# Optimization experiments

Measured on AMD Instinct MI355X. Metric: run time of the kernel, lower is better.

## Reference

```python
import jax, jax.numpy as jnp
import numpy as np

N, E, R, L = 20000, 160000, 3, 2
IN, HID, H, OUT = 64, 128, 16, 1
FH = HID // H   # per-head dim = 8
HD2 = HID // 2  # MLP bottleneck = 64


def setup_inputs() -> dict:
    key = jax.random.key(0)
    ks = iter(jax.random.split(key, 40))
    def w(*shape):
        return jax.random.normal(next(ks), shape, jnp.float32) * 0.05
    inp = dict(
        inputs=jax.random.normal(next(ks), (N, IN), jnp.float32),
        src=jax.random.randint(next(ks), (R, E), 0, N, dtype=jnp.int32),
        dst=jax.random.randint(next(ks), (R, E), 0, N, dtype=jnp.int32),
        e1_W=w(IN, HID), e1_b=jnp.zeros(HID), e_g=jnp.ones(HID), e_bt=jnp.zeros(HID),
        e2_W=w(HID, HID), e2_b=jnp.zeros(HID),
        gat_W=w(L, R, HID, HID), gat_al=w(L, R, H, FH), gat_ar=w(L, R, H, FH),
        gat_b=jnp.zeros((L, R, HID)),
        attn_p=w(L, R, HID),
        m1_W=w(L, HID, HD2), m1_b=jnp.zeros((L, HD2)), m_g=jnp.ones((L, HD2)), m_bt=jnp.zeros((L, HD2)),
        m2_W=w(L, HD2, HID), m2_b=jnp.zeros((L, HID)),
        d1_W=w(HID, HD2), d1_b=jnp.zeros(HD2), d_g=jnp.ones(HD2), d_bt=jnp.zeros(HD2),
        d2_W=w(HD2, OUT), d2_b=jnp.zeros(OUT),
    )
    return inp


def _bn(x, g, b):
    # BatchNorm1d, training mode: biased batch statistics, eps=1e-5
    mu = x.mean(0)
    var = jnp.mean((x - mu) ** 2, 0)
    return g * (x - mu) * jax.lax.rsqrt(var + 1e-5) + b


def _mlp(x, W1, b1, g, bt, W2, b2, skip=False):
    h = jax.nn.relu(_bn(x @ W1 + b1, g, bt))
    o = h @ W2 + b2
    return o + h if skip else o


def _gat(x, W, al, ar, b, src, dst):
    # single-relation DGL GATConv (feat_drop=attn_drop=0, neg_slope=0.2, bias)
    z = (x @ W).reshape(N, H, FH)                 # [N,H,FH]
    el = (z * al).sum(-1)                          # [N,H]
    er = (z * ar).sum(-1)                          # [N,H]
    e = jax.nn.leaky_relu(el[src] + er[dst], 0.2)  # [E,H]
    m = jax.ops.segment_max(e, dst, num_segments=N)
    m = jnp.where(jnp.isfinite(m), m, 0.0)
    ex = jnp.exp(e - m[dst])
    s = jax.ops.segment_sum(ex, dst, num_segments=N)
    alpha = ex / s[dst]                            # edge softmax over in-edges
    out = jax.ops.segment_sum(alpha[:, :, None] * z[src], dst, num_segments=N)
    return out.reshape(N, HID) + b                 # flatten heads + bias


def reference(inputs, src, dst, e1_W, e1_b, e_g, e_bt, e2_W, e2_b,
              gat_W, gat_al, gat_ar, gat_b, attn_p,
              m1_W, m1_b, m_g, m_bt, m2_W, m2_b,
              d1_W, d1_b, d_g, d_bt, d2_W, d2_b):
    h = _mlp(inputs, e1_W, e1_b, e_g, e_bt, e2_W, e2_b, skip=True)  # embed, skip
    gat_v = jax.vmap(_gat, in_axes=(None, 0, 0, 0, 0, 0, 0))        # over relations
    for l in range(L):
        stacked = gat_v(h, gat_W[l], gat_al[l], gat_ar[l], gat_b[l], src, dst)  # [R,N,HID]
        w = jax.nn.softmax(attn_p[l], axis=0)        # per-dim softmax over relations [R,HID]
        v = jnp.einsum('rnf,rf->nf', stacked, w)     # attn-weighted relation agg
        h = _mlp(v, m1_W[l], m1_b[l], m_g[l], m_bt[l], m2_W[l], m2_b[l]) + h
    return _mlp(h, d1_W, d1_b, d_g, d_bt, d2_W, d2_b)
```

## Files before the change

### kernel.cpp

```cpp
#include <hip/hip_runtime.h>
#include <math.h>

constexpr int kN   = 20000;
constexpr int kE   = 160000;
constexpr int kR   = 3;
constexpr int kL   = 2;
constexpr int kIN  = 64;
constexpr int kHID = 128;
constexpr int kH   = 16;
constexpr int kFH  = 8;
constexpr int kHD2 = 64;

typedef __bf16 bf16x8 __attribute__((ext_vector_type(8)));
typedef float  f32x4  __attribute__((ext_vector_type(4)));

__device__ __forceinline__ bf16x8 ldfrag(const __bf16* p) {
  return __builtin_bit_cast(bf16x8, *(const uint4*)p);
}
__device__ __forceinline__ f32x4 MF(bf16x8 a, bf16x8 b, f32x4 c) {
  return __builtin_amdgcn_mfma_f32_16x16x32_bf16(a, b, c, 0, 0, 0);
}

__device__ __forceinline__ void splitrow(const float* __restrict__ p, int koff,
                                         bool bn, const float* scS, const float* shS,
                                         bf16x8& hi, bf16x8& lo) {
  float4 xa = *(const float4*)(p + koff);
  float4 xb = *(const float4*)(p + koff + 4);
  float x[8] = {xa.x, xa.y, xa.z, xa.w, xb.x, xb.y, xb.z, xb.w};
  union { __bf16 b[8]; bf16x8 v; } uh, ul;
#pragma unroll
  for (int e = 0; e < 8; e++) {
    float y = x[e];
    if (bn) y = fmaxf(fmaf(y, scS[koff + e], shS[koff + e]), 0.f);
    __bf16 hb = (__bf16)y;
    uh.b[e] = hb;
    ul.b[e] = (__bf16)(y - (float)hb);
  }
  hi = uh.v; lo = ul.v;
}

template <int BP>
__global__ __launch_bounds__(256) void mgemm_kernel(
    const float* __restrict__ A, const __bf16* __restrict__ WT,
    const float* __restrict__ bias, const float* __restrict__ resf, int resmode,
    const float* __restrict__ bnstat, const float* __restrict__ bng,
    const float* __restrict__ bnbt, float invn,
    float* __restrict__ statS,
    float* __restrict__ Cf, __bf16* __restrict__ Chi,
    const float* __restrict__ alb, const float* __restrict__ arb,
    float* __restrict__ elb, float* __restrict__ erb,
    int n, int k, int m, long wstride, long cstride) {
  __shared__ __bf16 Bh[64][136];
  __shared__ __bf16 Bl[(BP == 3) ? 64 : 1][136];
  __shared__ float scS[128], shS[128];
  const int t  = threadIdx.x;
  const int w  = t >> 6;
  const int l  = t & 63;
  const int lr = l & 15;
  const int lg = l >> 4;
  const int rb = blockIdx.x * 64 + w * 16;
  const int c0 = blockIdx.y * 64;
  const __bf16* Whi = WT + (size_t)blockIdx.z * wstride;
  const __bf16* Wlo = Whi + (size_t)k * m;
  if (Chi) Chi += (size_t)blockIdx.z * cstride;
  const float* al = alb ? alb + blockIdx.z * kHID : nullptr;
  const float* ar = arb ? arb + blockIdx.z * kHID : nullptr;
  if (elb) { elb += blockIdx.z * 16; erb += blockIdx.z * 16; }

  const bool bn = bnstat != nullptr;
  if (bn && t < k) {
    float mu  = bnstat[t] * invn;
    float var = bnstat[k + t] * invn - mu * mu;
    float s = bng[t] * rsqrtf(var + 1e-5f);
    scS[t] = s; shS[t] = bnbt[t] - mu * s;
  }
  const int kseg = k >> 3;
  for (int idx = t; idx < 64 * kseg; idx += 256) {
    int col = idx / kseg, seg = idx - col * kseg;
    *(uint4*)&Bh[col][seg * 8] = *(const uint4*)&Whi[(size_t)(c0 + col) * k + seg * 8];
    if constexpr (BP == 3)
      *(uint4*)&Bl[col][seg * 8] = *(const uint4*)&Wlo[(size_t)(c0 + col) * k + seg * 8];
  }
  __syncthreads();

  int r0 = rb + lr; if (r0 > n - 1) r0 = n - 1;
  f32x4 acc[4] = {};

  for (int ks = 0; ks < (k >> 5); ks++) {
    const int koff = ks * 32 + lg * 8;
    bf16x8 a0h, a0l;
    splitrow(&A[(size_t)r0 * k], koff, bn, scS, shS, a0h, a0l);
#pragma unroll
    for (int j = 0; j < 4; j++) {
      bf16x8 bh = ldfrag(&Bh[j * 16 + lr][koff]);
      acc[j] = MF(a0h, bh, acc[j]);
      acc[j] = MF(a0l, bh, acc[j]);
      if constexpr (BP == 3) {
        bf16x8 bl = ldfrag(&Bl[j * 16 + lr][koff]);
        acc[j] = MF(a0h, bl, acc[j]);
      }
    }
  }

  float s[4] = {}, s2[4] = {};
#pragma unroll
  for (int q = 0; q < 4; q++) {
    int row = rb + lg * 4 + q;
    bool ok = row < n;
#pragma unroll
    for (int j = 0; j < 4; j++) {
      int col = c0 + j * 16 + lr;
      float v = acc[j][q];
      if (bias) v += bias[col];
      size_t off = (size_t)row * m + col;
      if (ok) {
        if (resmode == 1) v += resf[off];
        else if (resmode == 2) v += fmaxf(fmaf(resf[off], scS[col], shS[col]), 0.f);
        if (Cf) Cf[off] = v;
        if (Chi) Chi[off] = (__bf16)v;
        s[j] += v; s2[j] += v * v;
      }
    }
  }
  if (statS) {
    __syncthreads();
    float* red = (float*)&Bh[0][0];
#pragma unroll
    for (int j = 0; j < 4; j++) {
      float a = s[j], b = s2[j];
      a += __shfl_xor(a, 16, 64); a += __shfl_xor(a, 32, 64);
      b += __shfl_xor(b, 16, 64); b += __shfl_xor(b, 32, 64);
      if (lg == 0) { red[w * 64 + j * 16 + lr] = a; red[256 + w * 64 + j * 16 + lr] = b; }
    }
    __syncthreads();
    if (t < 64) {
      float a = red[t] + red[64 + t] + red[128 + t] + red[192 + t];
      float b = red[256 + t] + red[320 + t] + red[384 + t] + red[448 + t];
      atomicAdd(&statS[c0 + t], a);
      atomicAdd(&statS[m + c0 + t], b);
    }
  }
  if (al) {
#pragma unroll
    for (int q = 0; q < 4; q++) {
      int row = rb + lg * 4 + q;
#pragma unroll
      for (int j = 0; j < 4; j++) {
        int col = c0 + j * 16 + lr;
        float zv = acc[j][q];
        float pl = zv * al[col];
        float pr = zv * ar[col];
        pl += __shfl_xor(pl, 1, 64); pl += __shfl_xor(pl, 2, 64); pl += __shfl_xor(pl, 4, 64);
        pr += __shfl_xor(pr, 1, 64); pr += __shfl_xor(pr, 2, 64); pr += __shfl_xor(pr, 4, 64);
        if ((lr & 7) == 0 && row < n) {
          int hd = col >> 3;
          elb[((size_t)row << 6) + hd] = pl;
          erb[((size_t)row << 6) + hd] = pr;
        }
      }
    }
  }
}

struct WDesc { const float* src; long doff; int k, m; };
struct WDescs { WDesc d[13]; };
__global__ void prep_kernel(WDescs ds, __bf16* __restrict__ wt,
                            const int* __restrict__ dst, int* __restrict__ deg) {
  int y = blockIdx.y;
  if (y < 13) {
    WDesc dd = ds.d[y];
    int idx = blockIdx.x * 256 + threadIdx.x;
    if (idx >= dd.k * dd.m) return;
    int row = idx / dd.m, col = idx - row * dd.m;
    float v = dd.src[idx];
    __bf16 hb = (__bf16)v;
    __bf16 lb = (__bf16)(v - (float)hb);
    wt[dd.doff + (size_t)col * dd.k + row] = hb;
    wt[dd.doff + (size_t)dd.k * dd.m + (size_t)col * dd.k + row] = lb;
  } else {
    int r = y - 13;
    int e = blockIdx.x * 256 + threadIdx.x;
    if (e < kE) atomicAdd(&deg[r * kN + dst[r * kE + e]], 1);
  }
}

__global__ __launch_bounds__(1024) void csr_scan_kernel(const int* __restrict__ deg,
                                                        int* __restrict__ rowptr) {
  const int r = blockIdx.y;
  const int* dg = deg + r * kN;
  int* rp = rowptr + r * (kN + 1);
  const int t = threadIdx.x;
  constexpr int C = (kN + 1023) / 1024;
  const int base = t * C;
  int sum = 0;
#pragma unroll
  for (int i = 0; i < C; i++) {
    int j = base + i;
    if (j < kN) sum += dg[j];
  }
  __shared__ int warpTot[16];
  int lane = t & 63, wid = t >> 6;
  int v = sum;
  for (int off = 1; off < 64; off <<= 1) {
    int y = __shfl_up(v, off, 64);
    if (lane >= off) v += y;
  }
  if (lane == 63) warpTot[wid] = v;
  __syncthreads();
  int wadd = 0;
#pragma unroll
  for (int i = 0; i < 16; i++) if (i < wid) wadd += warpTot[i];
  int run = wadd + v - sum;
#pragma unroll
  for (int i = 0; i < C; i++) {
    int j = base + i;
    if (j < kN) { rp[j] = run; run += dg[j]; }
  }
  if (t == 1023) rp[kN] = run;
}

__global__ void scatter_kernel(const int* __restrict__ src, const int* __restrict__ dst,
                               const int* __restrict__ rowptr, int* __restrict__ cursor,
                               int* __restrict__ col) {
  int r = blockIdx.y;
  int e = blockIdx.x * 256 + threadIdx.x;
  if (e < kE) {
    int d = dst[r * kE + e];
    int p = atomicAdd(&cursor[r * kN + d], 1);
    col[r * kE + rowptr[r * (kN + 1) + d] + p] = src[r * kE + e];
  }
}

__global__ void gat3_kernel(const int* __restrict__ rowptr, const int* __restrict__ colidx,
                            const ushort* __restrict__ z, const float* __restrict__ elb,
                            const float* __restrict__ erb,
                            const float* __restrict__ attn_pl, const float* __restrict__ gat_bl,
                            float* __restrict__ vv) {
  __shared__ float wsmS[kR * kHID], cvecS[kHID];
  int t = threadIdx.x;
  if (t < kHID) {
    float p0 = attn_pl[t], p1 = attn_pl[kHID + t], p2 = attn_pl[2 * kHID + t];
    float mx = fmaxf(p0, fmaxf(p1, p2));
    float e0 = __expf(p0 - mx), e1 = __expf(p1 - mx), e2 = __expf(p2 - mx);
    float si = 1.f / (e0 + e1 + e2);
    wsmS[t] = e0 * si; wsmS[kHID + t] = e1 * si; wsmS[2 * kHID + t] = e2 * si;
    cvecS[t] = (e0 * gat_bl[t] + e1 * gat_bl[kHID + t] + e2 * gat_bl[2 * kHID + t]) * si;
  }
  __syncthreads();
  int idx = blockIdx.x * 256 + t;
  if (idx >= kN * kH) return;
  int d = idx >> 4, hh = idx & 15;
  const int fo = hh << 3;
  float out[kFH];
#pragma unroll
  for (int f = 0; f < kFH; f++) out[f] = cvecS[fo + f];
  for (int r = 0; r < kR; r++) {
    const int* rp = rowptr + r * (kN + 1);
    const int* ci = colidx + (size_t)r * kE;
    const ushort* zr = z + (size_t)r * kN * kHID;
    const int ro = r * 16 + hh;
    float erd = erb[((size_t)d << 6) + ro];
    int beg = rp[d], end = rp[d + 1];
    float s = 0.f;
    float acc[kFH] = {};
    for (int p = beg; p < end; p += 8) {
      int q[8]; float ev[8]; uint4 zz[8];
#pragma unroll
      for (int u = 0; u < 8; u++) {
        int pp = p + u;
        q[u] = ci[pp < end ? pp : end - 1];
      }
#pragma unroll
      for (int u = 0; u < 8; u++) ev[u] = elb[((size_t)q[u] << 6) + ro];
#pragma unroll
      for (int u = 0; u < 8; u++) zz[u] = *(const uint4*)(zr + ((size_t)q[u] << 7) + fo);
#pragma unroll
      for (int u = 0; u < 8; u++) {
        float v = ev[u] + erd;
        v = v > 0.f ? v : 0.2f * v;
        float ex = (p + u < end) ? __expf(v) : 0.f;
        s += ex;
        acc[0] = fmaf(ex, __uint_as_float(zz[u].x << 16),         acc[0]);
        acc[1] = fmaf(ex, __uint_as_float(zz[u].x & 0xffff0000u), acc[1]);
        acc[2] = fmaf(ex, __uint_as_float(zz[u].y << 16),         acc[2]);
        acc[3] = fmaf(ex, __uint_as_float(zz[u].y & 0xffff0000u), acc[3]);
        acc[4] = fmaf(ex, __uint_as_float(zz[u].z << 16),         acc[4]);
        acc[5] = fmaf(ex, __uint_as_float(zz[u].z & 0xffff0000u), acc[5]);
        acc[6] = fmaf(ex, __uint_as_float(zz[u].w << 16),         acc[6]);
        acc[7] = fmaf(ex, __uint_as_float(zz[u].w & 0xffff0000u), acc[7]);
      }
    }
    float inv = s > 0.f ? 1.f / s : 0.f;
    const float* wp = wsmS + r * kHID + fo;
#pragma unroll
    for (int f = 0; f < kFH; f++) out[f] = fmaf(wp[f] * inv, acc[f], out[f]);
  }
  float4* vp = (float4*)(vv + ((size_t)d << 7) + fo);
  vp[0] = make_float4(out[0], out[1], out[2], out[3]);
  vp[1] = make_float4(out[4], out[5], out[6], out[7]);
}

__global__ void gemv_out_kernel(const float* __restrict__ A, const float* __restrict__ statS,
                                const float* __restrict__ g, const float* __restrict__ bt,
                                float invn, const float* __restrict__ w,
                                const float* __restrict__ b, float* __restrict__ out,
                                int n, int k) {
  __shared__ float scS[kHD2], shS[kHD2];
  int t = threadIdx.x;
  if (t < k) {
    float mu  = statS[t] * invn;
    float var = statS[k + t] * invn - mu * mu;
    float s = g[t] * rsqrtf(var + 1e-5f);
    scS[t] = s; shS[t] = bt[t] - mu * s;
  }
  __syncthreads();
  int i = blockIdx.x * 256 + t;
  if (i >= n) return;
  const float4* a = (const float4*)(A + (size_t)i * k);
  float acc = b[0];
  for (int j4 = 0; j4 < k / 4; j4++) {
    float4 x = a[j4];
    int c = j4 * 4;
    acc = fmaf(fmaxf(fmaf(x.x, scS[c],     shS[c]),     0.f), w[c],     acc);
    acc = fmaf(fmaxf(fmaf(x.y, scS[c + 1], shS[c + 1]), 0.f), w[c + 1], acc);
    acc = fmaf(fmaxf(fmaf(x.z, scS[c + 2], shS[c + 2]), 0.f), w[c + 2], acc);
    acc = fmaf(fmaxf(fmaf(x.w, scS[c + 3], shS[c + 3]), 0.f), w[c + 3], acc);
  }
  out[i] = acc;
}

extern "C" void kernel_launch(void* const* d_in, const int* in_sizes, int n_in,
                              void* d_out, int out_size, void* d_ws, size_t ws_size,
                              hipStream_t stream) {
  const float* inputs = (const float*)d_in[0];
  const int*   src    = (const int*)d_in[1];
  const int*   dst    = (const int*)d_in[2];
  const float* e1_W   = (const float*)d_in[3];
  const float* e1_b   = (const float*)d_in[4];
  const float* e_g    = (const float*)d_in[5];
  const float* e_bt   = (const float*)d_in[6];
  const float* e2_W   = (const float*)d_in[7];
  const float* e2_b   = (const float*)d_in[8];
  const float* gat_W  = (const float*)d_in[9];
  const float* gat_al = (const float*)d_in[10];
  const float* gat_ar = (const float*)d_in[11];
  const float* gat_b  = (const float*)d_in[12];
  const float* attn_p = (const float*)d_in[13];
  const float* m1_W   = (const float*)d_in[14];
  const float* m1_b   = (const float*)d_in[15];
  const float* m_g    = (const float*)d_in[16];
  const float* m_bt   = (const float*)d_in[17];
  const float* m2_W   = (const float*)d_in[18];
  const float* m2_b   = (const float*)d_in[19];
  const float* d1_W   = (const float*)d_in[20];
  const float* d1_b   = (const float*)d_in[21];
  const float* d_g    = (const float*)d_in[22];
  const float* d_bt   = (const float*)d_in[23];
  const float* d2_W   = (const float*)d_in[24];
  const float* d2_b   = (const float*)d_in[25];

  float* ws = (float*)d_ws;
  size_t o = 0;
  float*  h     = ws + o; o += (size_t)kN * kHID;
  float*  bufA  = ws + o; o += (size_t)kN * kHID;
  float*  vv    = ws + o; o += (size_t)kN * kHID;
  float*  elbuf = ws + o; o += (size_t)kN * 64;
  float*  erbuf = ws + o; o += (size_t)kN * 64;
  __bf16* z     = (__bf16*)(ws + o); o += (size_t)kR * kN * kHID / 2;
  __bf16* wt    = (__bf16*)(ws + o); o += 327680 / 2;
  int* degcur   = (int*)(ws + o); o += (size_t)6 * kN;
  float* stats  = ws + o; o += 640;
  int* rowptr   = (int*)(ws + o); o += (size_t)kR * (kN + 1);
  int* colidx   = (int*)(ws + o); o += (size_t)kR * kE;
  (void)ws_size; (void)in_sizes; (void)n_in; (void)out_size;

  int* deg    = degcur;
  int* cursor = degcur + 3 * kN;
  float* stat_e1 = stats;
  float* stat_m1[2] = {stats + 256, stats + 384};
  float* stat_d1 = stats + 512;

  const long kWE1 = 0, kWE2 = 16384, kWZ = 49152;
  const long kWM1_0 = 245760, kWM1_1 = 262144, kWM2_0 = 278528, kWM2_1 = 294912, kWD1 = 311296;

  auto nb = [](long t) { return (int)((t + 255) / 256); };
  const dim3 gE(nb(kE), kR);
  const dim3 gP(nb(kE), 16);
  const dim3 gM128((kN + 63) / 64, 2, 1);
  const dim3 gM64((kN + 63) / 64, 1, 1);
  const dim3 gMZ((kN + 63) / 64, 2, kR);
  const float invn = 1.0f / kN;
  float* F0 = nullptr; const float* cF0 = nullptr;

  WDescs wd;
  wd.d[0] = {e1_W, kWE1, kIN, kHID};
  wd.d[1] = {e2_W, kWE2, kHID, kHID};
  for (int i = 0; i < 6; i++) wd.d[2 + i] = {gat_W + (size_t)i * 16384, kWZ + (long)i * 32768, kHID, kHID};
  wd.d[8]  = {m1_W,        kWM1_0, kHID, kHD2};
  wd.d[9]  = {m1_W + 8192, kWM1_1, kHID, kHD2};
  wd.d[10] = {m2_W,        kWM2_0, kHD2, kHID};
  wd.d[11] = {m2_W + 8192, kWM2_1, kHD2, kHID};
  wd.d[12] = {d1_W,        kWD1,   kHID, kHD2};
  hipMemsetAsync(degcur, 0, ((size_t)6 * kN + 640) * sizeof(int), stream);
  prep_kernel<<<gP, 256, 0, stream>>>(wd, wt, dst, deg);
  csr_scan_kernel<<<dim3(1, kR), 1024, 0, stream>>>(deg, rowptr);
  scatter_kernel<<<gE, 256, 0, stream>>>(src, dst, rowptr, cursor, colidx);

  mgemm_kernel<3><<<gM128, 256, 0, stream>>>(inputs, wt + kWE1, e1_b, cF0, 0,
                                          cF0, cF0, cF0, invn, stat_e1, bufA, nullptr,
                                          cF0, cF0, F0, F0, kN, kIN, kHID, 0, 0);
  mgemm_kernel<3><<<gM128, 256, 0, stream>>>(bufA, wt + kWE2, e2_b, bufA, 2,
                                          stat_e1, e_g, e_bt, invn, F0, h, nullptr,
                                          cF0, cF0, F0, F0, kN, kHID, kHID, 0, 0);

  for (int l = 0; l < kL; l++) {
    mgemm_kernel<2><<<gMZ, 256, 0, stream>>>(h, wt + kWZ + (long)l * 3 * 32768, cF0, cF0, 0,
                                          cF0, cF0, cF0, invn, F0, F0, z,
                                          gat_al + (size_t)l * kR * kHID,
                                          gat_ar + (size_t)l * kR * kHID, elbuf, erbuf,
                                          kN, kHID, kHID, 32768, (long)kN * kHID);
    gat3_kernel<<<nb((long)kN * kH), 256, 0, stream>>>(rowptr, colidx, (const ushort*)z,
                                             elbuf, erbuf,
                                             attn_p + (size_t)l * kR * kHID,
                                             gat_b + (size_t)l * kR * kHID, vv);
    mgemm_kernel<3><<<gM64, 256, 0, stream>>>(vv, wt + (l ? kWM1_1 : kWM1_0),
                                           m1_b + (size_t)l * kHD2, cF0, 0,
                                           cF0, cF0, cF0, invn, stat_m1[l], bufA, nullptr,
                                           cF0, cF0, F0, F0, kN, kHID, kHD2, 0, 0);
    mgemm_kernel<3><<<gM128, 256, 0, stream>>>(bufA, wt + (l ? kWM2_1 : kWM2_0),
                                            m2_b + (size_t)l * kHID, h, 1,
                                            stat_m1[l], m_g + (size_t)l * kHD2,
                                            m_bt + (size_t)l * kHD2, invn, F0, h, nullptr,
                                            cF0, cF0, F0, F0, kN, kHD2, kHID, 0, 0);
  }

  mgemm_kernel<3><<<gM64, 256, 0, stream>>>(h, wt + kWD1, d1_b, cF0, 0,
                                         cF0, cF0, cF0, invn, stat_d1, bufA, nullptr,
                                         cF0, cF0, F0, F0, kN, kHID, kHD2, 0, 0);
  gemv_out_kernel<<<nb(kN), 256, 0, stream>>>(bufA, stat_d1, d_g, d_bt, invn,
                                              d2_W, d2_b, (float*)d_out, kN, kHD2);
}
```

Measured before the change: 305.7 us.

## Split GAT aggregation across relations and sum partials in the following GEMM

The GAT aggregation kernel now launches one grid slice per relation instead of looping over all three relations per thread, giving three times the threads and shorter serial chains. Each relation writes its weighted partial output to a separate buffer, and the next MLP GEMM gains a SUM3 mode that loads the three partials and adds them before BN and the bf16 split. This exposes more parallelism for the latency-bound gather, at the cost of writing and re-reading two extra N×128 float buffers and some extra workspace.

```diff
diff --git a/kernel.cpp b/kernel.cpp
--- a/kernel.cpp
+++ b/kernel.cpp
@@ -21,25 +21,18 @@
   return __builtin_amdgcn_mfma_f32_16x16x32_bf16(a, b, c, 0, 0, 0);
 }
 
-__device__ __forceinline__ void splitrow(const float* __restrict__ p, int koff,
-                                         bool bn, const float* scS, const float* shS,
-                                         bf16x8& hi, bf16x8& lo) {
-  float4 xa = *(const float4*)(p + koff);
-  float4 xb = *(const float4*)(p + koff + 4);
-  float x[8] = {xa.x, xa.y, xa.z, xa.w, xb.x, xb.y, xb.z, xb.w};
+__device__ __forceinline__ void splitx(const float* x, bf16x8& hi, bf16x8& lo) {
   union { __bf16 b[8]; bf16x8 v; } uh, ul;
 #pragma unroll
   for (int e = 0; e < 8; e++) {
-    float y = x[e];
-    if (bn) y = fmaxf(fmaf(y, scS[koff + e], shS[koff + e]), 0.f);
-    __bf16 hb = (__bf16)y;
+    __bf16 hb = (__bf16)x[e];
     uh.b[e] = hb;
-    ul.b[e] = (__bf16)(y - (float)hb);
+    ul.b[e] = (__bf16)(x[e] - (float)hb);
   }
   hi = uh.v; lo = ul.v;
 }
 
-template <int BP>
+template <int BP, bool SUM3>
 __global__ __launch_bounds__(256) void mgemm_kernel(
     const float* __restrict__ A, const __bf16* __restrict__ WT,
     const float* __restrict__ bias, const float* __restrict__ resf, int resmode,
@@ -49,7 +42,7 @@
     float* __restrict__ Cf, __bf16* __restrict__ Chi,
     const float* __restrict__ alb, const float* __restrict__ arb,
     float* __restrict__ elb, float* __restrict__ erb,
-    int n, int k, int m, long wstride, long cstride) {
+    int n, int k, int m, long wstride, long cstride, long astride) {
   __shared__ __bf16 Bh[64][136];
   __shared__ __bf16 Bl[(BP == 3) ? 64 : 1][136];
   __shared__ float scS[128], shS[128];
@@ -88,8 +81,29 @@
 
   for (int ks = 0; ks < (k >> 5); ks++) {
     const int koff = ks * 32 + lg * 8;
+    const float* p0 = &A[(size_t)r0 * k + koff];
+    float x[8];
+    {
+      float4 xa = *(const float4*)p0;
+      float4 xb = *(const float4*)(p0 + 4);
+      x[0] = xa.x; x[1] = xa.y; x[2] = xa.z; x[3] = xa.w;
+      x[4] = xb.x; x[5] = xb.y; x[6] = xb.z; x[7] = xb.w;
+    }
+    if constexpr (SUM3) {
+      float4 ya = *(const float4*)(p0 + astride);
+      float4 yb = *(const float4*)(p0 + astride + 4);
+      float4 za = *(const float4*)(p0 + 2 * astride);
+      float4 zb = *(const float4*)(p0 + 2 * astride + 4);
+      x[0] += ya.x + za.x; x[1] += ya.y + za.y; x[2] += ya.z + za.z; x[3] += ya.w + za.w;
+      x[4] += yb.x + zb.x; x[5] += yb.y + zb.y; x[6] += yb.z + zb.z; x[7] += yb.w + zb.w;
+    }
+    if (bn) {
+#pragma unroll
+      for (int e = 0; e < 8; e++)
+        x[e] = fmaxf(fmaf(x[e], scS[koff + e], shS[koff + e]), 0.f);
+    }
     bf16x8 a0h, a0l;
-    splitrow(&A[(size_t)r0 * k], koff, bn, scS, shS, a0h, a0l);
+    splitx(x, a0h, a0l);
 #pragma unroll
     for (int j = 0; j < 4; j++) {
       bf16x8 bh = ldfrag(&Bh[j * 16 + lr][koff]);
@@ -235,67 +249,66 @@
                             const ushort* __restrict__ z, const float* __restrict__ elb,
                             const float* __restrict__ erb,
                             const float* __restrict__ attn_pl, const float* __restrict__ gat_bl,
-                            float* __restrict__ vv) {
-  __shared__ float wsmS[kR * kHID], cvecS[kHID];
+                            float* __restrict__ vvp) {
+  __shared__ float wpS[kHID], cvecS[kHID];
+  const int r = blockIdx.y;
   int t = threadIdx.x;
   if (t < kHID) {
     float p0 = attn_pl[t], p1 = attn_pl[kHID + t], p2 = attn_pl[2 * kHID + t];
     float mx = fmaxf(p0, fmaxf(p1, p2));
     float e0 = __expf(p0 - mx), e1 = __expf(p1 - mx), e2 = __expf(p2 - mx);
     float si = 1.f / (e0 + e1 + e2);
-    wsmS[t] = e0 * si; wsmS[kHID + t] = e1 * si; wsmS[2 * kHID + t] = e2 * si;
-    cvecS[t] = (e0 * gat_bl[t] + e1 * gat_bl[kHID + t] + e2 * gat_bl[2 * kHID + t]) * si;
+    float wr = (r == 0 ? e0 : r == 1 ? e1 : e2) * si;
+    wpS[t] = wr;
+    cvecS[t] = (r == 0) ? (e0 * gat_bl[t] + e1 * gat_bl[kHID + t] + e2 * gat_bl[2 * kHID + t]) * si
+                        : 0.f;
   }
   __syncthreads();
   int idx = blockIdx.x * 256 + t;
   if (idx >= kN * kH) return;
   int d = idx >> 4, hh = idx & 15;
   const int fo = hh << 3;
+  const int* rp = rowptr + r * (kN + 1);
+  const int* ci = colidx + (size_t)r * kE;
+  const ushort* zr = z + (size_t)r * kN * kHID;
+  const int ro = r * 16 + hh;
+  float erd = erb[((size_t)d << 6) + ro];
+  int beg = rp[d], end = rp[d + 1];
+  float s = 0.f;
+  float acc[kFH] = {};
+  for (int p = beg; p < end; p += 8) {
+    int q[8]; float ev[8]; uint4 zz[8];
+#pragma unroll
+    for (int u = 0; u < 8; u++) {
+      int pp = p + u;
+      q[u] = ci[pp < end ? pp : (end > beg ? end - 1 : 0)];
+    }
+#pragma unroll
+    for (int u = 0; u < 8; u++) ev[u] = elb[((size_t)q[u] << 6) + ro];
+#pragma unroll
+    for (int u = 0; u < 8; u++) zz[u] = *(const uint4*)(zr + ((size_t)q[u] << 7) + fo);
+#pragma unroll
+    for (int u = 0; u < 8; u++) {
+      float v = ev[u] + erd;
+      v = v > 0.f ? v : 0.2f * v;
+      float ex = (p + u < end) ? __expf(v) : 0.f;
+      s += ex;
+      acc[0] = fmaf(ex, __uint_as_float(zz[u].x << 16),         acc[0]);
+      acc[1] = fmaf(ex, __uint_as_float(zz[u].x & 0xffff0000u), acc[1]);
+      acc[2] = fmaf(ex, __uint_as_float(zz[u].y << 16),         acc[2]);
+      acc[3] = fmaf(ex, __uint_as_float(zz[u].y & 0xffff0000u), acc[3]);
+      acc[4] = fmaf(ex, __uint_as_float(zz[u].z << 16),         acc[4]);
+      acc[5] = fmaf(ex, __uint_as_float(zz[u].z & 0xffff0000u), acc[5]);
+      acc[6] = fmaf(ex, __uint_as_float(zz[u].w << 16),         acc[6]);
+      acc[7] = fmaf(ex, __uint_as_float(zz[u].w & 0xffff0000u), acc[7]);
+    }
+  }
+  float inv = s > 0.f ? 1.f / s : 0.f;
   float out[kFH];
 #pragma unroll
-  for (int f = 0; f < kFH; f++) out[f] = cvecS[fo + f];
-  for (int r = 0; r < kR; r++) {
-    const int* rp = rowptr + r * (kN + 1);
-    const int* ci = colidx + (size_t)r * kE;
-    const ushort* zr = z + (size_t)r * kN * kHID;
-    const int ro = r * 16 + hh;
-    float erd = erb[((size_t)d << 6) + ro];
-    int beg = rp[d], end = rp[d + 1];
-    float s = 0.f;
-    float acc[kFH] = {};
-    for (int p = beg; p < end; p += 8) {
-      int q[8]; float ev[8]; uint4 zz[8];
-#pragma unroll
-      for (int u = 0; u < 8; u++) {
-        int pp = p + u;
-        q[u] = ci[pp < end ? pp : end - 1];
-      }
-#pragma unroll
-      for (int u = 0; u < 8; u++) ev[u] = elb[((size_t)q[u] << 6) + ro];
-#pragma unroll
-      for (int u = 0; u < 8; u++) zz[u] = *(const uint4*)(zr + ((size_t)q[u] << 7) + fo);
-#pragma unroll
-      for (int u = 0; u < 8; u++) {
-        float v = ev[u] + erd;
-        v = v > 0.f ? v : 0.2f * v;
-        float ex = (p + u < end) ? __expf(v) : 0.f;
-        s += ex;
-        acc[0] = fmaf(ex, __uint_as_float(zz[u].x << 16),         acc[0]);
-        acc[1] = fmaf(ex, __uint_as_float(zz[u].x & 0xffff0000u), acc[1]);
-        acc[2] = fmaf(ex, __uint_as_float(zz[u].y << 16),         acc[2]);
-        acc[3] = fmaf(ex, __uint_as_float(zz[u].y & 0xffff0000u), acc[3]);
-        acc[4] = fmaf(ex, __uint_as_float(zz[u].z << 16),         acc[4]);
-        acc[5] = fmaf(ex, __uint_as_float(zz[u].z & 0xffff0000u), acc[5]);
-        acc[6] = fmaf(ex, __uint_as_float(zz[u].w << 16),         acc[6]);
-        acc[7] = fmaf(ex, __uint_as_float(zz[u].w & 0xffff0000u), acc[7]);
-      }
-    }
-    float inv = s > 0.f ? 1.f / s : 0.f;
-    const float* wp = wsmS + r * kHID + fo;
-#pragma unroll
-    for (int f = 0; f < kFH; f++) out[f] = fmaf(wp[f] * inv, acc[f], out[f]);
-  }
-  float4* vp = (float4*)(vv + ((size_t)d << 7) + fo);
+  for (int f = 0; f < kFH; f++)
+    out[f] = fmaf(wpS[fo + f] * inv, acc[f], cvecS[fo + f]);
+  float4* vp = (float4*)(vvp + (size_t)r * kN * kHID + ((size_t)d << 7) + fo);
   vp[0] = make_float4(out[0], out[1], out[2], out[3]);
   vp[1] = make_float4(out[4], out[5], out[6], out[7]);
 }
@@ -363,7 +376,7 @@
   size_t o = 0;
   float*  h     = ws + o; o += (size_t)kN * kHID;
   float*  bufA  = ws + o; o += (size_t)kN * kHID;
-  float*  vv    = ws + o; o += (size_t)kN * kHID;
+  float*  vvp   = ws + o; o += (size_t)kR * kN * kHID;
   float*  elbuf = ws + o; o += (size_t)kN * 64;
   float*  erbuf = ws + o; o += (size_t)kN * 64;
   __bf16* z     = (__bf16*)(ws + o); o += (size_t)kR * kN * kHID / 2;
@@ -389,6 +402,7 @@
   const dim3 gM128((kN + 63) / 64, 2, 1);
   const dim3 gM64((kN + 63) / 64, 1, 1);
   const dim3 gMZ((kN + 63) / 64, 2, kR);
+  const dim3 gG3(nb((long)kN * kH), kR);
   const float invn = 1.0f / kN;
   float* F0 = nullptr; const float* cF0 = nullptr;
 
@@ -406,37 +420,38 @@
   csr_scan_kernel<<<dim3(1, kR), 1024, 0, stream>>>(deg, rowptr);
   scatter_kernel<<<gE, 256, 0, stream>>>(src, dst, rowptr, cursor, colidx);
 
-  mgemm_kernel<3><<<gM128, 256, 0, stream>>>(inputs, wt + kWE1, e1_b, cF0, 0,
+  mgemm_kernel<3, false><<<gM128, 256, 0, stream>>>(inputs, wt + kWE1, e1_b, cF0, 0,
                                           cF0, cF0, cF0, invn, stat_e1, bufA, nullptr,
-                                          cF0, cF0, F0, F0, kN, kIN, kHID, 0, 0);
-  mgemm_kernel<3><<<gM128, 256, 0, stream>>>(bufA, wt + kWE2, e2_b, bufA, 2,
+                                          cF0, cF0, F0, F0, kN, kIN, kHID, 0, 0, 0);
+  mgemm_kernel<3, false><<<gM128, 256, 0, stream>>>(bufA, wt + kWE2, e2_b, bufA, 2,
                                           stat_e1, e_g, e_bt, invn, F0, h, nullptr,
-                                          cF0, cF0, F0, F0, kN, kHID, kHID, 0, 0);
+                                          cF0, cF0, F0, F0, kN, kHID, kHID, 0, 0, 0);
 
   for (int l = 0; l < kL; l++) {
-    mgemm_kernel<2><<<gMZ, 256, 0, stream>>>(h, wt + kWZ + (long)l * 3 * 32768, cF0, cF0, 0,
+    mgemm_kernel<2, false><<<gMZ, 256, 0, stream>>>(h, wt + kWZ + (long)l * 3 * 32768, cF0, cF0, 0,
                                           cF0, cF0, cF0, invn, F0, F0, z,
                                           gat_al + (size_t)l * kR * kHID,
                                           gat_ar + (size_t)l * kR * kHID, elbuf, erbuf,
-                                          kN, kHID, kHID, 32768, (long)kN * kHID);
-    gat3_kernel<<<nb((long)kN * kH), 256, 0, stream>>>(rowptr, colidx, (const ushort*)z,
+                                          kN, kHID, kHID, 32768, (long)kN * kHID, 0);
+    gat3_kernel<<<gG3, 256, 0, stream>>>(rowptr, colidx, (const ushort*)z,
                                              elbuf, erbuf,
                                              attn_p + (size_t)l * kR * kHID,
-                                             gat_b + (size_t)l * kR * kHID, vv);
-    mgemm_kernel<3><<<gM64, 256, 0, stream>>>(vv, wt + (l ? kWM1_1 : kWM1_0),
+                                             gat_b + (size_t)l * kR * kHID, vvp);
+    mgemm_kernel<3, true><<<gM64, 256, 0, stream>>>(vvp, wt + (l ? kWM1_1 : kWM1_0),
                                            m1_b + (size_t)l * kHD2, cF0, 0,
                                            cF0, cF0, cF0, invn, stat_m1[l], bufA, nullptr,
-                                           cF0, cF0, F0, F0, kN, kHID, kHD2, 0, 0);
-    mgemm_kernel<3><<<gM128, 256, 0, stream>>>(bufA, wt + (l ? kWM2_1 : kWM2_0),
+                                           cF0, cF0, F0, F0, kN, kHID, kHD2, 0, 0,
+                                           (long)kN * kHID);
+    mgemm_kernel<3, false><<<gM128, 256, 0, stream>>>(bufA, wt + (l ? kWM2_1 : kWM2_0),
                                             m2_b + (size_t)l * kHID, h, 1,
                                             stat_m1[l], m_g + (size_t)l * kHD2,
                                             m_bt + (size_t)l * kHD2, invn, F0, h, nullptr,
-                                            cF0, cF0, F0, F0, kN, kHD2, kHID, 0, 0);
-  }
-
-  mgemm_kernel<3><<<gM64, 256, 0, stream>>>(h, wt + kWD1, d1_b, cF0, 0,
+                                            cF0, cF0, F0, F0, kN, kHD2, kHID, 0, 0, 0);
+  }
+
+  mgemm_kernel<3, false><<<gM64, 256, 0, stream>>>(h, wt + kWD1, d1_b, cF0, 0,
                                          cF0, cF0, cF0, invn, stat_d1, bufA, nullptr,
-                                         cF0, cF0, F0, F0, kN, kHID, kHD2, 0, 0);
+                                         cF0, cF0, F0, F0, kN, kHID, kHD2, 0, 0, 0);
   gemv_out_kernel<<<nb(kN), 256, 0, stream>>>(bufA, stat_d1, d_g, d_bt, invn,
                                               d2_W, d2_b, (float*)d_out, kN, kHD2);
 }
```

Result: no change. 304.6 us (-0.3%).
